# Kernel optimization log

Hardware: AMD Instinct MI355X
Metric: run time of the kernel (lower is better)

The kernel has to match this reference:

```python
import jax, jax.numpy as jnp
import numpy as np

B, T, N, F_IN, F_OUT, K = 16, 12, 1024, 64, 64, 3


def setup_inputs() -> dict:
    key = jax.random.key(0)
    k1, k2, k3, k4 = jax.random.split(key, 4)
    x = jax.random.normal(k1, (B, T, N, F_IN), dtype=jnp.float32)
    spatial_attention = jax.random.uniform(k2, (B, N, N), dtype=jnp.float32)
    cheb = jax.random.normal(k3, (K, N, N), dtype=jnp.float32) / np.sqrt(N)
    # Xavier-uniform-ish init for Theta [K, F_in, F_out]
    limit = np.sqrt(6.0 / (F_IN + F_OUT))
    Theta = jax.random.uniform(k4, (K, F_IN, F_OUT), dtype=jnp.float32,
                               minval=-limit, maxval=limit)
    return {"x": x, "spatial_attention": spatial_attention, "cheb": cheb, "Theta": Theta}


def reference(x, spatial_attention, cheb, Theta):
    # Attention-weighted Chebyshev adjacencies: [B, K, N, N]
    A = cheb[None, :, :, :] * spatial_attention[:, None, :, :]
    # Graph propagation for all t, k at once: [B, T, K, N, F_in]
    rhs = jnp.einsum('bkij,btjf->btkif', A, x)
    # Per-order linear map + sum over K: [B, T, N, F_out]
    out = jnp.einsum('btkif,kfo->btio', rhs, Theta)
    return jax.nn.relu(out)
```

## Files before the change

### kernel.cpp

```cpp
#include <hip/hip_runtime.h>
#include <hip/hip_bf16.h>

#define BB 16
#define TT 12
#define NN 1024
#define FF 64
#define KC 3

typedef __bf16 bf16x8 __attribute__((ext_vector_type(8)));
typedef float  f32x4  __attribute__((ext_vector_type(4)));
typedef float  f32x16 __attribute__((ext_vector_type(16)));

#define A_BYTES (KC * 64 * 128)
#define X_BYTES (256 * 128)

__global__ __launch_bounds__(512, 2) void cheb_fused(
    const float* __restrict__ x,
    const float* __restrict__ att,
    const float* __restrict__ cheb,
    const float* __restrict__ Theta,
    float* __restrict__ out)
{
    __shared__ __align__(16) char lds_raw[A_BYTES + X_BYTES];
    char* Ab = lds_raw;
    char* Xb = lds_raw + A_BYTES;

    const int tid  = threadIdx.x;
    const int lane = tid & 63;
    const int wid  = tid >> 6;

    const int wg = (blockIdx.x & 7) * 96 + (blockIdx.x >> 3);
    const int b  = wg / 48;
    const int it = (wg % 48) / 3;
    const int tc = wg % 3;
    const int i_base = it * 64;
    const int t_base = tc * 4;

    const int wm  = wid >> 1;
    const int wn  = wid & 1;
    const int l31 = lane & 31;
    const int lg  = lane >> 5;
    const int sw3 = (l31 >> 2) & 7;

    const float* attB = att + (size_t)b * NN * NN;
    const float* xB   = x + (size_t)b * TT * NN * FF;

    const int r_a = tid >> 3;
    const int g_a = tid & 7;
    const int swza_st = ((r_a >> 2) & 7) << 4;
    int tl_s[4], jj_s[4], f_s[4], swzx_st[4];
    #pragma unroll
    for (int s = 0; s < 4; ++s) {
        int u   = tid + s * 512;
        tl_s[s] = u >> 9;
        int rem = u & 511;
        jj_s[s] = (rem >> 4) * 2;
        f_s[s]  = (rem & 15) * 4;
        swzx_st[s] = ((f_s[s] >> 2) & 7) << 4;
    }

    f32x4 ra0, ra1, rc0[KC], rc1[KC], rx0[4], rx1[4];

    auto load_tile = [&](int j0) {
        const float* ap = attB + (size_t)(i_base + r_a) * NN + j0 + g_a * 8;
        ra0 = *reinterpret_cast<const f32x4*>(ap);
        ra1 = *reinterpret_cast<const f32x4*>(ap + 4);
        #pragma unroll
        for (int k = 0; k < KC; ++k) {
            const float* cp = cheb + ((size_t)k * NN + i_base + r_a) * NN + j0 + g_a * 8;
            rc0[k] = *reinterpret_cast<const f32x4*>(cp);
            rc1[k] = *reinterpret_cast<const f32x4*>(cp + 4);
        }
        #pragma unroll
        for (int s = 0; s < 4; ++s) {
            const float* xp = xB + ((size_t)(t_base + tl_s[s]) * NN + j0 + jj_s[s]) * FF + f_s[s];
            rx0[s] = *reinterpret_cast<const f32x4*>(xp);
            rx1[s] = *reinterpret_cast<const f32x4*>(xp + FF);
        }
    };

    f32x16 acc[KC][2] = {};

    load_tile(0);
    for (int jt = 0; jt < NN / 64; ++jt) {
        __syncthreads();

        #pragma unroll
        for (int k = 0; k < KC; ++k) {
            bf16x8 w;
            #pragma unroll
            for (int e = 0; e < 4; ++e) {
                w[e]     = (__bf16)(rc0[k][e] * ra0[e]);
                w[e + 4] = (__bf16)(rc1[k][e] * ra1[e]);
            }
            *reinterpret_cast<bf16x8*>(Ab + (k * 64 + r_a) * 128 + ((g_a * 16) ^ swza_st)) = w;
        }
        #pragma unroll
        for (int s = 0; s < 4; ++s) {
            const int c0     = tl_s[s] * 64 + f_s[s];
            const int coloff = (jj_s[s] * 2) ^ swzx_st[s];
            #pragma unroll
            for (int e = 0; e < 4; ++e) {
                union { __bf16 h[2]; unsigned u32; } pk;
                pk.h[0] = (__bf16)rx0[s][e];
                pk.h[1] = (__bf16)rx1[s][e];
                *reinterpret_cast<unsigned*>(Xb + (c0 + e) * 128 + coloff) = pk.u32;
            }
        }
        __syncthreads();

        if (jt + 1 < NN / 64) load_tile((jt + 1) * 64);

        const int xrow0 = (wm * 64 + l31) * 128;
        const int xrow1 = xrow0 + 32 * 128;
        const int arow  = (wn * 32 + l31) * 128;
        #pragma unroll
        for (int kk = 0; kk < 4; ++kk) {
            const int off = ((kk * 2 + lg) ^ sw3) << 4;
            bf16x8 af0 = *reinterpret_cast<const bf16x8*>(Xb + xrow0 + off);
            bf16x8 af1 = *reinterpret_cast<const bf16x8*>(Xb + xrow1 + off);
            #pragma unroll
            for (int k = 0; k < KC; ++k) {
                bf16x8 bf = *reinterpret_cast<const bf16x8*>(Ab + k * 64 * 128 + arow + off);
                acc[k][0] = __builtin_amdgcn_mfma_f32_32x32x16_bf16(af0, bf, acc[k][0], 0, 0, 0);
                acc[k][1] = __builtin_amdgcn_mfma_f32_32x32x16_bf16(af1, bf, acc[k][1], 0, 0, 0);
            }
        }
    }

    __syncthreads();
    {
        const int fi0 = wid * 3;
        #pragma unroll
        for (int q = 0; q < 3; ++q) {
            int fi = fi0 + q;
            int k  = fi >> 3;
            int mo = (fi >> 2) & 1;
            int s  = fi & 3;
            int o  = 32 * mo + l31;
            int fb = 32 * (s >> 1) + 16 * (s & 1) + 4 * lg;
            bf16x8 v;
            #pragma unroll
            for (int e = 0; e < 8; ++e) {
                int f = fb + (e & 3) + 8 * (e >> 2);
                v[e] = (__bf16)Theta[(k * FF + f) * FF + o];
            }
            *reinterpret_cast<bf16x8*>(Xb + (fi * 64 + lane) * 16) = v;
        }
    }
    __syncthreads();

    f32x16 of[2] = {};
    #pragma unroll
    for (int k = 0; k < KC; ++k) {
        #pragma unroll
        for (int s = 0; s < 4; ++s) {
            bf16x8 pb;
            #pragma unroll
            for (int e = 0; e < 8; ++e)
                pb[e] = (__bf16)acc[k][s >> 1][e + 8 * (s & 1)];
            #pragma unroll
            for (int mo = 0; mo < 2; ++mo) {
                bf16x8 th = *reinterpret_cast<const bf16x8*>(
                    Xb + ((((k * 2 + mo) * 4 + s) * 64) + lane) * 16);
                of[mo] = __builtin_amdgcn_mfma_f32_32x32x16_bf16(pb, th, of[mo], 0, 0, 0);
            }
        }
    }

    const int t = t_base + wm;
    float* op = out + (((size_t)b * TT + t) * NN + i_base + wn * 32) * FF;
    #pragma unroll
    for (int mo = 0; mo < 2; ++mo) {
        #pragma unroll
        for (int r = 0; r < 16; ++r) {
            int row = (r & 3) + 8 * (r >> 2) + 4 * lg;
            int o   = 32 * mo + l31;
            float v = of[mo][r];
            op[(size_t)row * FF + o] = v > 0.0f ? v : 0.0f;
        }
    }
}

extern "C" void kernel_launch(void* const* d_in, const int* in_sizes, int n_in,
                              void* d_out, int out_size, void* d_ws, size_t ws_size,
                              hipStream_t stream) {
    const float* x     = (const float*)d_in[0];
    const float* att   = (const float*)d_in[1];
    const float* cheb  = (const float*)d_in[2];
    const float* Theta = (const float*)d_in[3];
    float* out = (float*)d_out;
    (void)d_ws; (void)ws_size; (void)in_sizes; (void)n_in; (void)out_size;

    dim3 grid(BB * (NN / 64) * (TT / 4));
    cheb_fused<<<grid, 512, 0, stream>>>(x, att, cheb, Theta, out);
}
```

Measured before the change: 128.5 us.

## Double-buffer LDS tiles and interleave staging stores with MFMA phases

Splits the shared-memory A and X tiles into two ping-pong buffers. Bf16 conversion and LDS stores for the next tile are interleaved between the MFMA phases of the current tile, which leaves one barrier per tile instead of two. MFMA bursts are wrapped in s_setprio to favour the matrix work. The cost is double the LDS footprint, which may stop two blocks from fitting on a CU as the launch bounds request, so occupancy can drop.

```diff
diff --git a/kernel.cpp b/kernel.cpp
--- a/kernel.cpp
+++ b/kernel.cpp
@@ -11,8 +11,10 @@
 typedef float  f32x4  __attribute__((ext_vector_type(4)));
 typedef float  f32x16 __attribute__((ext_vector_type(16)));
 
-#define A_BYTES (KC * 64 * 128)
-#define X_BYTES (256 * 128)
+#define A_TILE 24576
+#define X_TILE 32768
+
+#define MFMA_B(a, b, c) __builtin_amdgcn_mfma_f32_32x32x16_bf16(a, b, c, 0, 0, 0)
 
 __global__ __launch_bounds__(512, 2) void cheb_fused(
     const float* __restrict__ x,
@@ -21,9 +23,11 @@
     const float* __restrict__ Theta,
     float* __restrict__ out)
 {
-    __shared__ __align__(16) char lds_raw[A_BYTES + X_BYTES];
-    char* Ab = lds_raw;
-    char* Xb = lds_raw + A_BYTES;
+    __shared__ __align__(16) char lds_raw[2 * (A_TILE + X_TILE)];
+    char* Ab0 = lds_raw;
+    char* Xb0 = lds_raw + A_TILE;
+    char* Ab1 = lds_raw + A_TILE + X_TILE;
+    char* Xb1 = Ab1 + A_TILE;
 
     const int tid  = threadIdx.x;
     const int lane = tid & 63;
@@ -79,12 +83,7 @@
         }
     };
 
-    f32x16 acc[KC][2] = {};
-
-    load_tile(0);
-    for (int jt = 0; jt < NN / 64; ++jt) {
-        __syncthreads();
-
+    auto store_A = [&](char* Ab) {
         #pragma unroll
         for (int k = 0; k < KC; ++k) {
             bf16x8 w;
@@ -95,6 +94,9 @@
             }
             *reinterpret_cast<bf16x8*>(Ab + (k * 64 + r_a) * 128 + ((g_a * 16) ^ swza_st)) = w;
         }
+    };
+
+    auto store_X = [&](char* Xb) {
         #pragma unroll
         for (int s = 0; s < 4; ++s) {
             const int c0     = tl_s[s] * 64 + f_s[s];
@@ -107,28 +109,57 @@
                 *reinterpret_cast<unsigned*>(Xb + (c0 + e) * 128 + coloff) = pk.u32;
             }
         }
-        __syncthreads();
-
-        if (jt + 1 < NN / 64) load_tile((jt + 1) * 64);
-
-        const int xrow0 = (wm * 64 + l31) * 128;
-        const int xrow1 = xrow0 + 32 * 128;
-        const int arow  = (wn * 32 + l31) * 128;
-        #pragma unroll
-        for (int kk = 0; kk < 4; ++kk) {
-            const int off = ((kk * 2 + lg) ^ sw3) << 4;
-            bf16x8 af0 = *reinterpret_cast<const bf16x8*>(Xb + xrow0 + off);
-            bf16x8 af1 = *reinterpret_cast<const bf16x8*>(Xb + xrow1 + off);
-            #pragma unroll
-            for (int k = 0; k < KC; ++k) {
-                bf16x8 bf = *reinterpret_cast<const bf16x8*>(Ab + k * 64 * 128 + arow + off);
-                acc[k][0] = __builtin_amdgcn_mfma_f32_32x32x16_bf16(af0, bf, acc[k][0], 0, 0, 0);
-                acc[k][1] = __builtin_amdgcn_mfma_f32_32x32x16_bf16(af1, bf, acc[k][1], 0, 0, 0);
-            }
-        }
-    }
-
-    __syncthreads();
+    };
+
+    f32x16 acc[KC][2] = {};
+    const int xrow0 = (wm * 64 + l31) * 128;
+    const int xrow1 = xrow0 + 32 * 128;
+    const int arow  = (wn * 32 + l31) * 128;
+
+    auto phase = [&](const char* AbR, const char* XbR, int kk) {
+        const int off = ((kk * 2 + lg) ^ sw3) << 4;
+        bf16x8 af0 = *reinterpret_cast<const bf16x8*>(XbR + xrow0 + off);
+        bf16x8 af1 = *reinterpret_cast<const bf16x8*>(XbR + xrow1 + off);
+        bf16x8 b0  = *reinterpret_cast<const bf16x8*>(AbR + arow + off);
+        bf16x8 b1  = *reinterpret_cast<const bf16x8*>(AbR + 8192 + arow + off);
+        bf16x8 b2  = *reinterpret_cast<const bf16x8*>(AbR + 16384 + arow + off);
+        __builtin_amdgcn_s_setprio(1);
+        acc[0][0] = MFMA_B(af0, b0, acc[0][0]); acc[0][1] = MFMA_B(af1, b0, acc[0][1]);
+        acc[1][0] = MFMA_B(af0, b1, acc[1][0]); acc[1][1] = MFMA_B(af1, b1, acc[1][1]);
+        acc[2][0] = MFMA_B(af0, b2, acc[2][0]); acc[2][1] = MFMA_B(af1, b2, acc[2][1]);
+        __builtin_amdgcn_s_setprio(0);
+    };
+
+    load_tile(0);
+    store_A(Ab0);
+    store_X(Xb0);
+    load_tile(64);
+    asm volatile("s_waitcnt lgkmcnt(0)" ::: "memory");
+    __builtin_amdgcn_s_barrier();
+
+    for (int jt2 = 0; jt2 < 8; ++jt2) {
+        const int jt = jt2 * 2;
+        phase(Ab0, Xb0, 0);
+        phase(Ab0, Xb0, 1);
+        store_A(Ab1);
+        phase(Ab0, Xb0, 2);
+        store_X(Xb1);
+        phase(Ab0, Xb0, 3);
+        if (jt + 2 < 16) load_tile((jt + 2) * 64);
+        asm volatile("s_waitcnt lgkmcnt(0)" ::: "memory");
+        __builtin_amdgcn_s_barrier();
+
+        phase(Ab1, Xb1, 0);
+        phase(Ab1, Xb1, 1);
+        if (jt + 1 < 15) store_A(Ab0);
+        phase(Ab1, Xb1, 2);
+        if (jt + 1 < 15) store_X(Xb0);
+        phase(Ab1, Xb1, 3);
+        if (jt + 3 < 16) load_tile((jt + 3) * 64);
+        asm volatile("s_waitcnt lgkmcnt(0)" ::: "memory");
+        __builtin_amdgcn_s_barrier();
+    }
+
     {
         const int fi0 = wid * 3;
         #pragma unroll
@@ -145,7 +176,7 @@
                 int f = fb + (e & 3) + 8 * (e >> 2);
                 v[e] = (__bf16)Theta[(k * FF + f) * FF + o];
             }
-            *reinterpret_cast<bf16x8*>(Xb + (fi * 64 + lane) * 16) = v;
+            *reinterpret_cast<bf16x8*>(lds_raw + (fi * 64 + lane) * 16) = v;
         }
     }
     __syncthreads();
@@ -162,8 +193,8 @@
             #pragma unroll
             for (int mo = 0; mo < 2; ++mo) {
                 bf16x8 th = *reinterpret_cast<const bf16x8*>(
-                    Xb + ((((k * 2 + mo) * 4 + s) * 64) + lane) * 16);
-                of[mo] = __builtin_amdgcn_mfma_f32_32x32x16_bf16(pb, th, of[mo], 0, 0, 0);
+                    lds_raw + ((((k * 2 + mo) * 4 + s) * 64) + lane) * 16);
+                of[mo] = MFMA_B(pb, th, of[mo]);
             }
         }
     }
```

Result: no change. 127.1 us (-1.1%).
